# Kernel optimization log

Measured on AMD Instinct MI355X. Metric: run time of the kernel, lower is better.

The kernel has to match this reference:

```python
import jax, jax.numpy as jnp
import numpy as np

IN, H, NE, ED = 2048, 1024, 1024, 8
BETA = 0.001
LN_EPS = 1e-5


def _ln(x, g, b):
    m = jnp.mean(x, axis=-1, keepdims=True)
    v = jnp.var(x, axis=-1, keepdims=True)
    return (x - m) / jnp.sqrt(v + LN_EPS) * g + b


def setup_inputs() -> dict:
    key = jax.random.key(0)
    ks = jax.random.split(key, 10)

    def lin(k, fan_in, fan_out):
        lim = 1.0 / np.sqrt(fan_in)
        k1, k2 = jax.random.split(k)
        W = jax.random.uniform(k1, (fan_in, fan_out), minval=-lim, maxval=lim, dtype=jnp.float32)
        b = jax.random.uniform(k2, (fan_out,), minval=-lim, maxval=lim, dtype=jnp.float32)
        return W, b

    x = jax.random.normal(ks[0], (4096, IN), dtype=jnp.float32)
    r = ED ** -0.5
    codebook = jax.random.uniform(ks[1], (NE, ED), minval=-r, maxval=r, dtype=jnp.float32)
    W0, b0 = lin(ks[2], IN, H)
    W1, b1 = lin(ks[3], H, H)
    W2, b2 = lin(ks[4], H, H)
    W3, b3 = lin(ks[5], H, H)
    W4, b4 = lin(ks[6], H, H)
    W5, b5 = lin(ks[7], H, IN)
    ones = jnp.ones((H,), jnp.float32)
    zeros = jnp.zeros((H,), jnp.float32)
    return {
        "x": x, "codebook": codebook,
        "W0": W0, "b0": b0, "g0": ones, "be0": zeros,
        "W1": W1, "b1": b1, "g1": ones, "be1": zeros,
        "W2": W2, "b2": b2, "g2": ones, "be2": zeros,
        "W3": W3, "b3": b3, "g3": ones, "be3": zeros,
        "W4": W4, "b4": b4, "g4": ones, "be4": zeros,
        "W5": W5, "b5": b5,
    }


def reference(x, codebook,
              W0, b0, g0, be0,
              W1, b1, g1, be1,
              W2, b2, g2, be2,
              W3, b3, g3, be3,
              W4, b4, g4, be4,
              W5, b5):
    # encoder: Linear -> LN -> ReLU (x2) -> Linear -> LN
    h = jax.nn.relu(_ln(x @ W0 + b0, g0, be0))
    h = jax.nn.relu(_ln(h @ W1 + b1, g1, be1))
    z = _ln(h @ W2 + b2, g2, be2)                      # [B, H]

    # vector quantize: cdist^2 -> argmin -> gather, straight-through
    zf = z.reshape(-1, ED)                             # [B*H/ED, ED]
    d = (jnp.sum(zf * zf, axis=1, keepdims=True)
         + jnp.sum(codebook * codebook, axis=1)
         - 2.0 * zf @ codebook.T)                      # [B*H/ED, NE]
    idx = jnp.argmin(d, axis=1)
    z_q = codebook[idx].reshape(z.shape)
    loss = (jnp.mean((jax.lax.stop_gradient(z_q) - z) ** 2)
            + BETA * jnp.mean((z_q - jax.lax.stop_gradient(z)) ** 2))
    z_q = z + jax.lax.stop_gradient(z_q - z)

    # decoder: ReLU -> Linear -> LN (x2 with ReLU) -> ReLU -> Linear
    h = jax.nn.relu(z_q)
    h = jax.nn.relu(_ln(h @ W3 + b3, g3, be3))
    h = jax.nn.relu(_ln(h @ W4 + b4, g4, be4))
    x_hat = h @ W5 + b5
    return x_hat, loss
```

## Files before the change

kernel.cpp:

```cpp
#include <hip/hip_runtime.h>

namespace {

constexpr int BATCH = 4096;
constexpr int DIN   = 2048;
constexpr int HID   = 1024;
constexpr int NEMB  = 1024;
constexpr int EDIM  = 8;
constexpr float LN_EPS = 1e-5f;
constexpr float BETA   = 0.001f;

typedef __attribute__((ext_vector_type(8))) short bf16x8;
typedef __attribute__((ext_vector_type(4))) float f32x4;

__device__ inline unsigned short f2bf(float f) {
  unsigned int x = __float_as_uint(f);
  x += 0x7FFFu + ((x >> 16) & 1u);
  return (unsigned short)(x >> 16);
}
__device__ inline void gl16(const void* g, void* l) {
  __builtin_amdgcn_global_load_lds(
      (const __attribute__((address_space(1))) unsigned int*)g,
      (__attribute__((address_space(3))) unsigned int*)l, 16, 0, 0);
}

__global__ __launch_bounds__(256) void gemm_f32_sk(
    const float* __restrict__ A, const float* __restrict__ B,
    float* __restrict__ P, int M, int N, int K)
{
  constexpr int BM = 128, BN = 128, BK = 16;
  __shared__ float As[BK][BM + 4];
  __shared__ float Bs[BK][BN];
  const int t  = threadIdx.x;
  const int tx = t & 15, ty = t >> 4;
  const int bm = blockIdx.y * BM, bn = blockIdx.x * BN;
  const int Kh = K >> 1, kbeg = blockIdx.z * Kh;
  float* Pz = P + (size_t)blockIdx.z * M * N;

  const int a_m = t >> 1, a_k = (t & 1) << 3;
  const int b_k = t >> 4, b_n = (t & 15) << 3;

  const float* Ap = A + (size_t)(bm + a_m) * K + kbeg + a_k;
  const float* Bp = B + (size_t)(kbeg + b_k) * N + (bn + b_n);

  float acc[8][8] = {};

  for (int k0 = 0; k0 < Kh; k0 += BK) {
    float4 av0 = *(const float4*)(Ap + k0);
    float4 av1 = *(const float4*)(Ap + k0 + 4);
    float4 bv0 = *(const float4*)(Bp + (size_t)k0 * N);
    float4 bv1 = *(const float4*)(Bp + (size_t)k0 * N + 4);
    __syncthreads();
    As[a_k + 0][a_m] = av0.x;
    As[a_k + 1][a_m] = av0.y;
    As[a_k + 2][a_m] = av0.z;
    As[a_k + 3][a_m] = av0.w;
    As[a_k + 4][a_m] = av1.x;
    As[a_k + 5][a_m] = av1.y;
    As[a_k + 6][a_m] = av1.z;
    As[a_k + 7][a_m] = av1.w;
    *(float4*)&Bs[b_k][b_n]     = bv0;
    *(float4*)&Bs[b_k][b_n + 4] = bv1;
    __syncthreads();

    float part[8][8] = {};
#pragma unroll
    for (int k = 0; k < BK; ++k) {
      float a[8], b[8];
      *(float4*)(a)     = *(const float4*)&As[k][ty * 8];
      *(float4*)(a + 4) = *(const float4*)&As[k][ty * 8 + 4];
      *(float4*)(b)     = *(const float4*)&Bs[k][tx * 8];
      *(float4*)(b + 4) = *(const float4*)&Bs[k][tx * 8 + 4];
#pragma unroll
      for (int i = 0; i < 8; ++i)
#pragma unroll
        for (int j = 0; j < 8; ++j)
          part[i][j] = fmaf(a[i], b[j], part[i][j]);
    }
#pragma unroll
    for (int i = 0; i < 8; ++i)
#pragma unroll
      for (int j = 0; j < 8; ++j)
        acc[i][j] += part[i][j];
  }

#pragma unroll
  for (int i = 0; i < 8; ++i) {
    float* Pr = Pz + (size_t)(bm + ty * 8 + i) * N + bn + tx * 8;
    *(float4*)(Pr)     = *(float4*)&acc[i][0];
    *(float4*)(Pr + 4) = *(float4*)&acc[i][4];
  }
}

template<bool RELU>
__global__ __launch_bounds__(256) void ln_sk(
    const float* __restrict__ P0, const float* __restrict__ P1,
    const float* __restrict__ bias, float* __restrict__ Y,
    const float* __restrict__ g, const float* __restrict__ be)
{
  const int t = threadIdx.x;
  const size_t base = (size_t)blockIdx.x * HID + t * 4;
  float4 p0 = *(const float4*)(P0 + base);
  float4 p1 = *(const float4*)(P1 + base);
  float4 bb = *(const float4*)(bias + t * 4);
  float4 v;
  v.x = (p0.x + p1.x) + bb.x;
  v.y = (p0.y + p1.y) + bb.y;
  v.z = (p0.z + p1.z) + bb.z;
  v.w = (p0.w + p1.w) + bb.w;
  float s = v.x + v.y + v.z + v.w;
  float q = v.x * v.x + v.y * v.y + v.z * v.z + v.w * v.w;
#pragma unroll
  for (int off = 32; off > 0; off >>= 1) {
    s += __shfl_down(s, off);
    q += __shfl_down(q, off);
  }
  __shared__ float ls[4], lq[4];
  if ((t & 63) == 0) { ls[t >> 6] = s; lq[t >> 6] = q; }
  __syncthreads();
  s = ls[0] + ls[1] + ls[2] + ls[3];
  q = lq[0] + lq[1] + lq[2] + lq[3];
  const float mean = s * (1.0f / HID);
  const float var  = q * (1.0f / HID) - mean * mean;
  const float rstd = rsqrtf(var + LN_EPS);
  float4 gv = *(const float4*)(g + t * 4);
  float4 bv = *(const float4*)(be + t * 4);
  float4 o;
  o.x = (v.x - mean) * rstd * gv.x + bv.x;
  o.y = (v.y - mean) * rstd * gv.y + bv.y;
  o.z = (v.z - mean) * rstd * gv.z + bv.z;
  o.w = (v.w - mean) * rstd * gv.w + bv.w;
  if (RELU) {
    o.x = fmaxf(o.x, 0.0f); o.y = fmaxf(o.y, 0.0f);
    o.z = fmaxf(o.z, 0.0f); o.w = fmaxf(o.w, 0.0f);
  }
  *(float4*)(Y + base) = o;
}

__global__ __launch_bounds__(256) void gemm_mfma(
    const unsigned short* __restrict__ Ah, const unsigned short* __restrict__ Bh,
    const float* __restrict__ bias, float* __restrict__ C,
    int M, int N, int K)
{
  constexpr int BM = 128, BN = 64, BK = 64;
  __shared__ unsigned short lds[(BM + BN) * BK];
  const int t = threadIdx.x, l = t & 63, w = t >> 6;
  const int wr = w >> 1, wc = w & 1;
  const int m0 = blockIdx.y * BM, n0 = blockIdx.x * BN;
  const int NT = K / BK;

  const int AHo = 0, BHo = BM * BK * 2;

  const int srow = t >> 3, scol = t & 7;
  size_t aoff[4]; int adst[4];
#pragma unroll
  for (int i = 0; i < 4; ++i) {
    int r = srow + 32 * i;
    aoff[i] = (size_t)(m0 + r) * K + ((scol ^ (r & 7)) << 3);
    adst[i] = r * 128 + scol * 16;
  }
  size_t boff[2]; int bdst[2];
#pragma unroll
  for (int i = 0; i < 2; ++i) {
    int r = srow + 32 * i;
    boff[i] = (size_t)(n0 + r) * K + ((scol ^ (r & 7)) << 3);
    bdst[i] = r * 128 + scol * 16;
  }
  char* lc = (char*)lds;

  auto GLOAD = [&](int tk) {
    const size_t k0 = (size_t)tk * BK;
#pragma unroll
    for (int i = 0; i < 4; ++i) gl16(Ah + aoff[i] + k0, lc + AHo + adst[i]);
#pragma unroll
    for (int i = 0; i < 2; ++i) gl16(Bh + boff[i] + k0, lc + BHo + bdst[i]);
  };

  f32x4 acc[4][2];
#pragma unroll
  for (int i = 0; i < 4; ++i)
#pragma unroll
    for (int j = 0; j < 2; ++j) acc[i][j] = 0.0f;

  const int l15 = l & 15, kb0 = l >> 4;
  const int swz = (l15 & 7) << 4;
  int arow[4], brow[2];
#pragma unroll
  for (int fm = 0; fm < 4; ++fm) arow[fm] = (wr * 64 + fm * 16 + l15) * 128;
#pragma unroll
  for (int fn = 0; fn < 2; ++fn) brow[fn] = (wc * 32 + fn * 16 + l15) * 128;

  GLOAD(0);
  for (int tk = 0; tk < NT; ++tk) {
    __syncthreads();
    const char* p = (const char*)lds;
#pragma unroll
    for (int kh = 0; kh < 2; ++kh) {
      const int kby = (kh * 64 + kb0 * 16) ^ swz;
      bf16x8 af[4], bf2[2];
#pragma unroll
      for (int fm = 0; fm < 4; ++fm)
        af[fm] = *(const bf16x8*)(p + AHo + arow[fm] + kby);
#pragma unroll
      for (int fn = 0; fn < 2; ++fn)
        bf2[fn] = *(const bf16x8*)(p + BHo + brow[fn] + kby);
#pragma unroll
      for (int fm = 0; fm < 4; ++fm)
#pragma unroll
        for (int fn = 0; fn < 2; ++fn)
          acc[fm][fn] = __builtin_amdgcn_mfma_f32_16x16x32_bf16(
              af[fm], bf2[fn], acc[fm][fn], 0, 0, 0);
    }
    __syncthreads();
    if (tk + 1 < NT) GLOAD(tk + 1);
  }

  const int rb = (l >> 4) * 4;
#pragma unroll
  for (int fn = 0; fn < 2; ++fn) {
    const int n = n0 + wc * 32 + fn * 16 + l15;
    const float bv = bias[n];
#pragma unroll
    for (int fm = 0; fm < 4; ++fm) {
      const int m = m0 + wr * 64 + fm * 16 + rb;
      float* Cp = C + (size_t)m * N + n;
#pragma unroll
      for (int ri = 0; ri < 4; ++ri)
        Cp[(size_t)ri * N] = acc[fm][fn][ri] + bv;
    }
  }
}

__global__ __launch_bounds__(256) void conv_w_t(
    const float* __restrict__ W, unsigned short* __restrict__ Wt, int K, int N)
{
  __shared__ float tile[32][33];
  const int tx = threadIdx.x & 31, ty = threadIdx.x >> 5;
  const int n0 = blockIdx.x * 32, k0 = blockIdx.y * 32;
#pragma unroll
  for (int r = ty; r < 32; r += 8)
    tile[r][tx] = W[(size_t)(k0 + r) * N + n0 + tx];
  __syncthreads();
#pragma unroll
  for (int r = ty; r < 32; r += 8)
    Wt[(size_t)(n0 + r) * K + k0 + tx] = f2bf(tile[tx][r]);
}

template<bool RELU>
__global__ __launch_bounds__(256) void ln_act(
    const float* __restrict__ X, unsigned short* __restrict__ Y,
    const float* __restrict__ g, const float* __restrict__ be)
{
  const int t = threadIdx.x;
  const size_t base = (size_t)blockIdx.x * HID + t * 4;
  float4 v = *(const float4*)(X + base);
  float s = v.x + v.y + v.z + v.w;
  float q = v.x * v.x + v.y * v.y + v.z * v.z + v.w * v.w;
#pragma unroll
  for (int off = 32; off > 0; off >>= 1) {
    s += __shfl_down(s, off);
    q += __shfl_down(q, off);
  }
  __shared__ float ls[4], lq[4];
  if ((t & 63) == 0) { ls[t >> 6] = s; lq[t >> 6] = q; }
  __syncthreads();
  s = ls[0] + ls[1] + ls[2] + ls[3];
  q = lq[0] + lq[1] + lq[2] + lq[3];
  const float mean = s * (1.0f / HID);
  const float var  = q * (1.0f / HID) - mean * mean;
  const float rstd = rsqrtf(var + LN_EPS);
  float4 gv = *(const float4*)(g + t * 4);
  float4 bv = *(const float4*)(be + t * 4);
  float4 o;
  o.x = (v.x - mean) * rstd * gv.x + bv.x;
  o.y = (v.y - mean) * rstd * gv.y + bv.y;
  o.z = (v.z - mean) * rstd * gv.z + bv.z;
  o.w = (v.w - mean) * rstd * gv.w + bv.w;
  if (RELU) {
    o.x = fmaxf(o.x, 0.0f); o.y = fmaxf(o.y, 0.0f);
    o.z = fmaxf(o.z, 0.0f); o.w = fmaxf(o.w, 0.0f);
  }
  ushort4 u = { f2bf(o.x), f2bf(o.y), f2bf(o.z), f2bf(o.w) };
  *(ushort4*)(Y + base) = u;
}

__global__ __launch_bounds__(256) void vq_kernel(
    const float* __restrict__ Z, const float* __restrict__ CB,
    unsigned short* __restrict__ ZQb, float* __restrict__ partial)
{
  __shared__ float e[NEMB][EDIM];
  __shared__ float qn[NEMB];
  const int t = threadIdx.x;
  for (int i = t; i < NEMB * EDIM / 4; i += 256)
    ((float4*)&e[0][0])[i] = ((const float4*)CB)[i];
  __syncthreads();
  for (int i = t; i < NEMB; i += 256) {
    float s = 0.0f;
#pragma unroll
    for (int j = 0; j < EDIM; ++j) s += e[i][j] * e[i][j];
    qn[i] = 0.5f * s;
  }
  __syncthreads();

  constexpr int R = 2;
  size_t sv[R];
  float z[R][EDIM];
#pragma unroll
  for (int r = 0; r < R; ++r) {
    sv[r] = (size_t)blockIdx.x * 512 + t + 256 * r;
    *(float4*)(z[r])     = *(const float4*)(Z + sv[r] * EDIM);
    *(float4*)(z[r] + 4) = *(const float4*)(Z + sv[r] * EDIM + 4);
  }

  float b1[R], b2[R];
  int   i1[R], i2[R];
#pragma unroll
  for (int r = 0; r < R; ++r) { b1[r] = 1e30f; b2[r] = 1e30f; i1[r] = 0; i2[r] = 0; }

  for (int i = 0; i < NEMB; i += 4) {
    const float4 qv = *(const float4*)&qn[i];
#pragma unroll
    for (int u = 0; u < 4; ++u) {
      const float4 e0 = *(const float4*)&e[i + u][0];
      const float4 e1 = *(const float4*)&e[i + u][4];
      const float q = (u == 0) ? qv.x : (u == 1) ? qv.y : (u == 2) ? qv.z : qv.w;
      const int ii = i + u;
#pragma unroll
      for (int r = 0; r < R; ++r) {
        float d = q;
        d = fmaf(-z[r][0], e0.x, d);
        d = fmaf(-z[r][1], e0.y, d);
        d = fmaf(-z[r][2], e0.z, d);
        d = fmaf(-z[r][3], e0.w, d);
        d = fmaf(-z[r][4], e1.x, d);
        d = fmaf(-z[r][5], e1.y, d);
        d = fmaf(-z[r][6], e1.z, d);
        d = fmaf(-z[r][7], e1.w, d);
        const bool lt1 = d < b1[r];
        const bool lt2 = d < b2[r];
        i2[r] = lt1 ? i1[r] : (lt2 ? ii : i2[r]);
        b2[r] = fminf(fmaxf(d, b1[r]), b2[r]);
        if (lt1) { b1[r] = d; i1[r] = ii; }
      }
    }
  }

  double lsum = 0.0;
#pragma unroll
  for (int r = 0; r < R; ++r) {
    if (b2[r] - b1[r] < 1e-3f) {
      double d1 = 0.0, d2 = 0.0;
#pragma unroll
      for (int j = 0; j < EDIM; ++j) {
        double f1 = (double)z[r][j] - (double)e[i1[r]][j];
        double f2 = (double)z[r][j] - (double)e[i2[r]][j];
        d1 += f1 * f1; d2 += f2 * f2;
      }
      if (d2 < d1 || (d2 == d1 && i2[r] < i1[r])) i1[r] = i2[r];
    }
    double lq = 0.0;
#pragma unroll
    for (int j = 0; j < EDIM; ++j) {
      double diff = (double)z[r][j] - (double)e[i1[r]][j];
      lq += diff * diff;
    }
    lsum += lq;

    float o[EDIM];
#pragma unroll
    for (int j = 0; j < EDIM; ++j) o[j] = fmaxf(e[i1[r]][j], 0.0f);
    uint4 pk;
    pk.x = (unsigned)f2bf(o[0]) | ((unsigned)f2bf(o[1]) << 16);
    pk.y = (unsigned)f2bf(o[2]) | ((unsigned)f2bf(o[3]) << 16);
    pk.z = (unsigned)f2bf(o[4]) | ((unsigned)f2bf(o[5]) << 16);
    pk.w = (unsigned)f2bf(o[6]) | ((unsigned)f2bf(o[7]) << 16);
    *(uint4*)(ZQb + sv[r] * EDIM) = pk;
  }

#pragma unroll
  for (int off = 32; off > 0; off >>= 1) lsum += __shfl_down(lsum, off);
  __shared__ double lsh[4];
  if ((t & 63) == 0) lsh[t >> 6] = lsum;
  __syncthreads();
  if (t == 0) partial[blockIdx.x] = (float)(lsh[0] + lsh[1] + lsh[2] + lsh[3]);
}

__global__ __launch_bounds__(256) void loss_finalize(
    const float* __restrict__ partial, float* __restrict__ out)
{
  const int t = threadIdx.x;
  double s = 0.0;
  for (int i = t; i < 1024; i += 256) s += (double)partial[i];
#pragma unroll
  for (int off = 32; off > 0; off >>= 1) s += __shfl_down(s, off);
  __shared__ double ls[4];
  if ((t & 63) == 0) ls[t >> 6] = s;
  __syncthreads();
  if (t == 0) {
    double total = ls[0] + ls[1] + ls[2] + ls[3];
    out[0] = (float)(total * (1.0 + (double)BETA) / (double)((size_t)BATCH * HID));
  }
}

}

extern "C" void kernel_launch(void* const* d_in, const int* in_sizes, int n_in,
                              void* d_out, int out_size, void* d_ws, size_t ws_size,
                              hipStream_t stream)
{
  const float* x   = (const float*)d_in[0];
  const float* cb  = (const float*)d_in[1];
  const float* W0  = (const float*)d_in[2];
  const float* b0  = (const float*)d_in[3];
  const float* g0  = (const float*)d_in[4];
  const float* be0 = (const float*)d_in[5];
  const float* W1  = (const float*)d_in[6];
  const float* b1  = (const float*)d_in[7];
  const float* g1  = (const float*)d_in[8];
  const float* be1 = (const float*)d_in[9];
  const float* W2  = (const float*)d_in[10];
  const float* b2  = (const float*)d_in[11];
  const float* g2  = (const float*)d_in[12];
  const float* be2 = (const float*)d_in[13];
  const float* W3  = (const float*)d_in[14];
  const float* b3  = (const float*)d_in[15];
  const float* g3  = (const float*)d_in[16];
  const float* be3 = (const float*)d_in[17];
  const float* W4  = (const float*)d_in[18];
  const float* b4  = (const float*)d_in[19];
  const float* g4  = (const float*)d_in[20];
  const float* be4 = (const float*)d_in[21];
  const float* W5  = (const float*)d_in[22];
  const float* b5  = (const float*)d_in[23];
  float* out = (float*)d_out;

  char* ws = (char*)d_ws;
  constexpr size_t MB = 1024 * 1024;
  float* C32 = (float*)ws;
  float* Q   = (float*)(ws + 16 * MB);
  unsigned short* Qb  = (unsigned short*)(ws + 16 * MB);
  unsigned short* W3H = (unsigned short*)(ws + 24 * MB);
  unsigned short* W4H = (unsigned short*)(ws + 26 * MB);
  unsigned short* W5H = (unsigned short*)(ws + 28 * MB);
  float* partial = (float*)(ws + 32 * MB);
  float* P0 = (float*)d_out;
  float* P1 = (float*)((char*)d_out + 16 * MB);
  float* Z  = (float*)((char*)d_out + 16 * MB);

  dim3 blk(256);
  dim3 gSK(HID / 128, BATCH / 128, 2);
  dim3 gDH(HID / 64, BATCH / 128);
  dim3 gDO(DIN / 64, BATCH / 128);

  gemm_f32_sk<<<gSK, blk, 0, stream>>>(x, W0, P0, BATCH, HID, DIN);
  ln_sk<true><<<dim3(BATCH), blk, 0, stream>>>(P0, P1, b0, Q, g0, be0);
  gemm_f32_sk<<<gSK, blk, 0, stream>>>(Q, W1, P0, BATCH, HID, HID);
  ln_sk<true><<<dim3(BATCH), blk, 0, stream>>>(P0, P1, b1, Q, g1, be1);
  gemm_f32_sk<<<gSK, blk, 0, stream>>>(Q, W2, P0, BATCH, HID, HID);
  ln_sk<false><<<dim3(BATCH), blk, 0, stream>>>(P0, P1, b2, Z, g2, be2);

  conv_w_t<<<dim3(HID / 32, HID / 32), blk, 0, stream>>>(W3, W3H, HID, HID);
  conv_w_t<<<dim3(HID / 32, HID / 32), blk, 0, stream>>>(W4, W4H, HID, HID);
  conv_w_t<<<dim3(DIN / 32, HID / 32), blk, 0, stream>>>(W5, W5H, HID, DIN);

  vq_kernel<<<dim3(1024), blk, 0, stream>>>(Z, cb, Qb, partial);

  gemm_mfma<<<gDH, blk, 0, stream>>>(Qb, W3H, b3, C32, BATCH, HID, HID);
  ln_act<true><<<dim3(BATCH), blk, 0, stream>>>(C32, Qb, g3, be3);
  gemm_mfma<<<gDH, blk, 0, stream>>>(Qb, W4H, b4, C32, BATCH, HID, HID);
  ln_act<true><<<dim3(BATCH), blk, 0, stream>>>(C32, Qb, g4, be4);
  gemm_mfma<<<gDO, blk, 0, stream>>>(Qb, W5H, b5, out, BATCH, DIN, HID);

  loss_finalize<<<dim3(1), blk, 0, stream>>>(partial, out + (size_t)BATCH * DIN);
}
```

Baseline: 816.8 us.

## Use 3-way split-K for fp32 encoder GEMMs and halve VQ shared memory

The fp32 encoder GEMMs now split K three ways instead of two. The grid goes from 512 to 768 blocks, which gives better wave fill on 256 CUs, and the third partial is written to the C32 workspace; the LayerNorm kernels now sum three partials. The VQ kernel loads the codebook in two halves so it needs half the LDS, which raises occupancy, and it fetches the chosen codewords from global memory for the loss and output. The cost is extra partial-buffer traffic and extra barriers in the VQ kernel.

```diff
diff --git a/kernel.cpp b/kernel.cpp
--- a/kernel.cpp
+++ b/kernel.cpp
@@ -26,7 +26,8 @@
 
 __global__ __launch_bounds__(256) void gemm_f32_sk(
     const float* __restrict__ A, const float* __restrict__ B,
-    float* __restrict__ P, int M, int N, int K)
+    float* __restrict__ P0, float* __restrict__ P1, float* __restrict__ P2,
+    int M, int N, int K)
 {
   constexpr int BM = 128, BN = 128, BK = 16;
   __shared__ float As[BK][BM + 4];
@@ -34,8 +35,12 @@
   const int t  = threadIdx.x;
   const int tx = t & 15, ty = t >> 4;
   const int bm = blockIdx.y * BM, bn = blockIdx.x * BN;
-  const int Kh = K >> 1, kbeg = blockIdx.z * Kh;
-  float* Pz = P + (size_t)blockIdx.z * M * N;
+  const int zz = blockIdx.z;
+  const int ntile = K >> 4, q = ntile / 3, rr = ntile % 3;
+  const int myt  = q + (zz < rr ? 1 : 0);
+  const int kbeg = (zz * q + (zz < rr ? zz : rr)) << 4;
+  const int Kh   = myt << 4;
+  float* Pz = (zz == 0) ? P0 : (zz == 1) ? P1 : P2;
 
   const int a_m = t >> 1, a_k = (t & 1) << 3;
   const int b_k = t >> 4, b_n = (t & 15) << 3;
@@ -93,21 +98,23 @@
 }
 
 template<bool RELU>
-__global__ __launch_bounds__(256) void ln_sk(
+__global__ __launch_bounds__(256) void ln_sk3(
     const float* __restrict__ P0, const float* __restrict__ P1,
-    const float* __restrict__ bias, float* __restrict__ Y,
+    const float* __restrict__ P2, const float* __restrict__ bias,
+    float* __restrict__ Y,
     const float* __restrict__ g, const float* __restrict__ be)
 {
   const int t = threadIdx.x;
   const size_t base = (size_t)blockIdx.x * HID + t * 4;
   float4 p0 = *(const float4*)(P0 + base);
   float4 p1 = *(const float4*)(P1 + base);
+  float4 p2 = *(const float4*)(P2 + base);
   float4 bb = *(const float4*)(bias + t * 4);
   float4 v;
-  v.x = (p0.x + p1.x) + bb.x;
-  v.y = (p0.y + p1.y) + bb.y;
-  v.z = (p0.z + p1.z) + bb.z;
-  v.w = (p0.w + p1.w) + bb.w;
+  v.x = ((p0.x + p1.x) + p2.x) + bb.x;
+  v.y = ((p0.y + p1.y) + p2.y) + bb.y;
+  v.z = ((p0.z + p1.z) + p2.z) + bb.z;
+  v.w = ((p0.w + p1.w) + p2.w) + bb.w;
   float s = v.x + v.y + v.z + v.w;
   float q = v.x * v.x + v.y * v.y + v.z * v.z + v.w * v.w;
 #pragma unroll
@@ -288,19 +295,10 @@
     const float* __restrict__ Z, const float* __restrict__ CB,
     unsigned short* __restrict__ ZQb, float* __restrict__ partial)
 {
-  __shared__ float e[NEMB][EDIM];
-  __shared__ float qn[NEMB];
+  constexpr int HN = NEMB / 2;
+  __shared__ float e[HN][EDIM];
+  __shared__ float qn[HN];
   const int t = threadIdx.x;
-  for (int i = t; i < NEMB * EDIM / 4; i += 256)
-    ((float4*)&e[0][0])[i] = ((const float4*)CB)[i];
-  __syncthreads();
-  for (int i = t; i < NEMB; i += 256) {
-    float s = 0.0f;
-#pragma unroll
-    for (int j = 0; j < EDIM; ++j) s += e[i][j] * e[i][j];
-    qn[i] = 0.5f * s;
-  }
-  __syncthreads();
 
   constexpr int R = 2;
   size_t sv[R];
@@ -317,30 +315,45 @@
 #pragma unroll
   for (int r = 0; r < R; ++r) { b1[r] = 1e30f; b2[r] = 1e30f; i1[r] = 0; i2[r] = 0; }
 
-  for (int i = 0; i < NEMB; i += 4) {
-    const float4 qv = *(const float4*)&qn[i];
-#pragma unroll
-    for (int u = 0; u < 4; ++u) {
-      const float4 e0 = *(const float4*)&e[i + u][0];
-      const float4 e1 = *(const float4*)&e[i + u][4];
-      const float q = (u == 0) ? qv.x : (u == 1) ? qv.y : (u == 2) ? qv.z : qv.w;
-      const int ii = i + u;
-#pragma unroll
-      for (int r = 0; r < R; ++r) {
-        float d = q;
-        d = fmaf(-z[r][0], e0.x, d);
-        d = fmaf(-z[r][1], e0.y, d);
-        d = fmaf(-z[r][2], e0.z, d);
-        d = fmaf(-z[r][3], e0.w, d);
-        d = fmaf(-z[r][4], e1.x, d);
-        d = fmaf(-z[r][5], e1.y, d);
-        d = fmaf(-z[r][6], e1.z, d);
-        d = fmaf(-z[r][7], e1.w, d);
-        const bool lt1 = d < b1[r];
-        const bool lt2 = d < b2[r];
-        i2[r] = lt1 ? i1[r] : (lt2 ? ii : i2[r]);
-        b2[r] = fminf(fmaxf(d, b1[r]), b2[r]);
-        if (lt1) { b1[r] = d; i1[r] = ii; }
+  for (int half = 0; half < 2; ++half) {
+    if (half) __syncthreads();
+    for (int i = t; i < HN * EDIM / 4; i += 256)
+      ((float4*)&e[0][0])[i] = ((const float4*)(CB + (size_t)half * HN * EDIM))[i];
+    __syncthreads();
+    for (int i = t; i < HN; i += 256) {
+      float s = 0.0f;
+#pragma unroll
+      for (int j = 0; j < EDIM; ++j) s += e[i][j] * e[i][j];
+      qn[i] = 0.5f * s;
+    }
+    __syncthreads();
+
+    const int ibase = half * HN;
+    for (int i = 0; i < HN; i += 4) {
+      const float4 qv = *(const float4*)&qn[i];
+#pragma unroll
+      for (int u = 0; u < 4; ++u) {
+        const float4 e0 = *(const float4*)&e[i + u][0];
+        const float4 e1 = *(const float4*)&e[i + u][4];
+        const float q = (u == 0) ? qv.x : (u == 1) ? qv.y : (u == 2) ? qv.z : qv.w;
+        const int ii = ibase + i + u;
+#pragma unroll
+        for (int r = 0; r < R; ++r) {
+          float d = q;
+          d = fmaf(-z[r][0], e0.x, d);
+          d = fmaf(-z[r][1], e0.y, d);
+          d = fmaf(-z[r][2], e0.z, d);
+          d = fmaf(-z[r][3], e0.w, d);
+          d = fmaf(-z[r][4], e1.x, d);
+          d = fmaf(-z[r][5], e1.y, d);
+          d = fmaf(-z[r][6], e1.z, d);
+          d = fmaf(-z[r][7], e1.w, d);
+          const bool lt1 = d < b1[r];
+          const bool lt2 = d < b2[r];
+          i2[r] = lt1 ? i1[r] : (lt2 ? ii : i2[r]);
+          b2[r] = fminf(fmaxf(d, b1[r]), b2[r]);
+          if (lt1) { b1[r] = d; i1[r] = ii; }
+        }
       }
     }
   }
@@ -348,32 +361,38 @@
   double lsum = 0.0;
 #pragma unroll
   for (int r = 0; r < R; ++r) {
+    float c1[EDIM], c2[EDIM];
+    *(float4*)(c1)     = *(const float4*)(CB + (size_t)i1[r] * EDIM);
+    *(float4*)(c1 + 4) = *(const float4*)(CB + (size_t)i1[r] * EDIM + 4);
     if (b2[r] - b1[r] < 1e-3f) {
+      *(float4*)(c2)     = *(const float4*)(CB + (size_t)i2[r] * EDIM);
+      *(float4*)(c2 + 4) = *(const float4*)(CB + (size_t)i2[r] * EDIM + 4);
       double d1 = 0.0, d2 = 0.0;
 #pragma unroll
       for (int j = 0; j < EDIM; ++j) {
-        double f1 = (double)z[r][j] - (double)e[i1[r]][j];
-        double f2 = (double)z[r][j] - (double)e[i2[r]][j];
+        double f1 = (double)z[r][j] - (double)c1[j];
+        double f2 = (double)z[r][j] - (double)c2[j];
         d1 += f1 * f1; d2 += f2 * f2;
       }
-      if (d2 < d1 || (d2 == d1 && i2[r] < i1[r])) i1[r] = i2[r];
+      if (d2 < d1 || (d2 == d1 && i2[r] < i1[r])) {
+        i1[r] = i2[r];
+#pragma unroll
+        for (int j = 0; j < EDIM; ++j) c1[j] = c2[j];
+      }
     }
     double lq = 0.0;
 #pragma unroll
     for (int j = 0; j < EDIM; ++j) {
-      double diff = (double)z[r][j] - (double)e[i1[r]][j];
+      double diff = (double)z[r][j] - (double)c1[j];
       lq += diff * diff;
     }
     lsum += lq;
 
-    float o[EDIM];
-#pragma unroll
-    for (int j = 0; j < EDIM; ++j) o[j] = fmaxf(e[i1[r]][j], 0.0f);
     uint4 pk;
-    pk.x = (unsigned)f2bf(o[0]) | ((unsigned)f2bf(o[1]) << 16);
-    pk.y = (unsigned)f2bf(o[2]) | ((unsigned)f2bf(o[3]) << 16);
-    pk.z = (unsigned)f2bf(o[4]) | ((unsigned)f2bf(o[5]) << 16);
-    pk.w = (unsigned)f2bf(o[6]) | ((unsigned)f2bf(o[7]) << 16);
+    pk.x = (unsigned)f2bf(fmaxf(c1[0], 0.0f)) | ((unsigned)f2bf(fmaxf(c1[1], 0.0f)) << 16);
+    pk.y = (unsigned)f2bf(fmaxf(c1[2], 0.0f)) | ((unsigned)f2bf(fmaxf(c1[3], 0.0f)) << 16);
+    pk.z = (unsigned)f2bf(fmaxf(c1[4], 0.0f)) | ((unsigned)f2bf(fmaxf(c1[5], 0.0f)) << 16);
+    pk.w = (unsigned)f2bf(fmaxf(c1[6], 0.0f)) | ((unsigned)f2bf(fmaxf(c1[7], 0.0f)) << 16);
     *(uint4*)(ZQb + sv[r] * EDIM) = pk;
   }
 
@@ -448,16 +467,16 @@
   float* Z  = (float*)((char*)d_out + 16 * MB);
 
   dim3 blk(256);
-  dim3 gSK(HID / 128, BATCH / 128, 2);
+  dim3 gSK(HID / 128, BATCH / 128, 3);
   dim3 gDH(HID / 64, BATCH / 128);
   dim3 gDO(DIN / 64, BATCH / 128);
 
-  gemm_f32_sk<<<gSK, blk, 0, stream>>>(x, W0, P0, BATCH, HID, DIN);
-  ln_sk<true><<<dim3(BATCH), blk, 0, stream>>>(P0, P1, b0, Q, g0, be0);
-  gemm_f32_sk<<<gSK, blk, 0, stream>>>(Q, W1, P0, BATCH, HID, HID);
-  ln_sk<true><<<dim3(BATCH), blk, 0, stream>>>(P0, P1, b1, Q, g1, be1);
-  gemm_f32_sk<<<gSK, blk, 0, stream>>>(Q, W2, P0, BATCH, HID, HID);
-  ln_sk<false><<<dim3(BATCH), blk, 0, stream>>>(P0, P1, b2, Z, g2, be2);
+  gemm_f32_sk<<<gSK, blk, 0, stream>>>(x, W0, P0, P1, C32, BATCH, HID, DIN);
+  ln_sk3<true><<<dim3(BATCH), blk, 0, stream>>>(P0, P1, C32, b0, Q, g0, be0);
+  gemm_f32_sk<<<gSK, blk, 0, stream>>>(Q, W1, P0, P1, C32, BATCH, HID, HID);
+  ln_sk3<true><<<dim3(BATCH), blk, 0, stream>>>(P0, P1, C32, b1, Q, g1, be1);
+  gemm_f32_sk<<<gSK, blk, 0, stream>>>(Q, W2, P0, P1, C32, BATCH, HID, HID);
+  ln_sk3<false><<<dim3(BATCH), blk, 0, stream>>>(P0, P1, C32, b2, Z, g2, be2);
 
   conv_w_t<<<dim3(HID / 32, HID / 32), blk, 0, stream>>>(W3, W3H, HID, HID);
   conv_w_t<<<dim3(HID / 32, HID / 32), blk, 0, stream>>>(W4, W4H, HID, HID);
```

Measured after the change: 826.9 us. About the same (+1.2%).

## Halve VQ codebook LDS footprint and process one vector per thread

Applied to the files above, without the earlier changes.

The VQ kernel now stages the codebook in shared memory in two halves of 512 entries instead of all 1024. Each thread handles one vector instead of two, and the grid doubles to 2048 blocks. The final codeword values are read from global memory rather than LDS. The intent is lower LDS use per block (about 18KB instead of 36KB) and more parallelism, for higher occupancy in the distance-scan loop. In exchange, each block loads and normalises the codebook per half, adds extra barriers, and the loss partial reduction covers twice as many entries.

```diff
diff --git a/kernel.cpp b/kernel.cpp
--- a/kernel.cpp
+++ b/kernel.cpp
@@ -288,94 +288,91 @@
     const float* __restrict__ Z, const float* __restrict__ CB,
     unsigned short* __restrict__ ZQb, float* __restrict__ partial)
 {
-  __shared__ float e[NEMB][EDIM];
-  __shared__ float qn[NEMB];
+  constexpr int HN = NEMB / 2;
+  __shared__ float e[HN][EDIM];
+  __shared__ float qn[HN];
   const int t = threadIdx.x;
-  for (int i = t; i < NEMB * EDIM / 4; i += 256)
-    ((float4*)&e[0][0])[i] = ((const float4*)CB)[i];
-  __syncthreads();
-  for (int i = t; i < NEMB; i += 256) {
-    float s = 0.0f;
-#pragma unroll
-    for (int j = 0; j < EDIM; ++j) s += e[i][j] * e[i][j];
-    qn[i] = 0.5f * s;
-  }
-  __syncthreads();
-
-  constexpr int R = 2;
-  size_t sv[R];
-  float z[R][EDIM];
-#pragma unroll
-  for (int r = 0; r < R; ++r) {
-    sv[r] = (size_t)blockIdx.x * 512 + t + 256 * r;
-    *(float4*)(z[r])     = *(const float4*)(Z + sv[r] * EDIM);
-    *(float4*)(z[r] + 4) = *(const float4*)(Z + sv[r] * EDIM + 4);
-  }
-
-  float b1[R], b2[R];
-  int   i1[R], i2[R];
-#pragma unroll
-  for (int r = 0; r < R; ++r) { b1[r] = 1e30f; b2[r] = 1e30f; i1[r] = 0; i2[r] = 0; }
-
-  for (int i = 0; i < NEMB; i += 4) {
-    const float4 qv = *(const float4*)&qn[i];
-#pragma unroll
-    for (int u = 0; u < 4; ++u) {
-      const float4 e0 = *(const float4*)&e[i + u][0];
-      const float4 e1 = *(const float4*)&e[i + u][4];
-      const float q = (u == 0) ? qv.x : (u == 1) ? qv.y : (u == 2) ? qv.z : qv.w;
-      const int ii = i + u;
-#pragma unroll
-      for (int r = 0; r < R; ++r) {
+
+  const size_t sv = (size_t)blockIdx.x * 256 + t;
+  float z[EDIM];
+  *(float4*)(z)     = *(const float4*)(Z + sv * EDIM);
+  *(float4*)(z + 4) = *(const float4*)(Z + sv * EDIM + 4);
+
+  float b1 = 1e30f, b2 = 1e30f;
+  int   i1 = 0, i2 = 0;
+
+  for (int half = 0; half < 2; ++half) {
+    if (half) __syncthreads();
+    for (int i = t; i < HN * EDIM / 4; i += 256)
+      ((float4*)&e[0][0])[i] = ((const float4*)(CB + (size_t)half * HN * EDIM))[i];
+    __syncthreads();
+    for (int i = t; i < HN; i += 256) {
+      float s = 0.0f;
+#pragma unroll
+      for (int j = 0; j < EDIM; ++j) s += e[i][j] * e[i][j];
+      qn[i] = 0.5f * s;
+    }
+    __syncthreads();
+
+    const int ibase = half * HN;
+    for (int i = 0; i < HN; i += 4) {
+      const float4 qv = *(const float4*)&qn[i];
+#pragma unroll
+      for (int u = 0; u < 4; ++u) {
+        const float4 e0 = *(const float4*)&e[i + u][0];
+        const float4 e1 = *(const float4*)&e[i + u][4];
+        const float q = (u == 0) ? qv.x : (u == 1) ? qv.y : (u == 2) ? qv.z : qv.w;
+        const int ii = ibase + i + u;
         float d = q;
-        d = fmaf(-z[r][0], e0.x, d);
-        d = fmaf(-z[r][1], e0.y, d);
-        d = fmaf(-z[r][2], e0.z, d);
-        d = fmaf(-z[r][3], e0.w, d);
-        d = fmaf(-z[r][4], e1.x, d);
-        d = fmaf(-z[r][5], e1.y, d);
-        d = fmaf(-z[r][6], e1.z, d);
-        d = fmaf(-z[r][7], e1.w, d);
-        const bool lt1 = d < b1[r];
-        const bool lt2 = d < b2[r];
-        i2[r] = lt1 ? i1[r] : (lt2 ? ii : i2[r]);
-        b2[r] = fminf(fmaxf(d, b1[r]), b2[r]);
-        if (lt1) { b1[r] = d; i1[r] = ii; }
+        d = fmaf(-z[0], e0.x, d);
+        d = fmaf(-z[1], e0.y, d);
+        d = fmaf(-z[2], e0.z, d);
+        d = fmaf(-z[3], e0.w, d);
+        d = fmaf(-z[4], e1.x, d);
+        d = fmaf(-z[5], e1.y, d);
+        d = fmaf(-z[6], e1.z, d);
+        d = fmaf(-z[7], e1.w, d);
+        const bool lt1 = d < b1;
+        const bool lt2 = d < b2;
+        i2 = lt1 ? i1 : (lt2 ? ii : i2);
+        b2 = fminf(fmaxf(d, b1), b2);
+        if (lt1) { b1 = d; i1 = ii; }
       }
     }
   }
 
+  float c1[EDIM], c2[EDIM];
+  *(float4*)(c1)     = *(const float4*)(CB + (size_t)i1 * EDIM);
+  *(float4*)(c1 + 4) = *(const float4*)(CB + (size_t)i1 * EDIM + 4);
+  if (b2 - b1 < 1e-3f) {
+    *(float4*)(c2)     = *(const float4*)(CB + (size_t)i2 * EDIM);
+    *(float4*)(c2 + 4) = *(const float4*)(CB + (size_t)i2 * EDIM + 4);
+    double d1 = 0.0, d2 = 0.0;
+#pragma unroll
+    for (int j = 0; j < EDIM; ++j) {
+      double f1 = (double)z[j] - (double)c1[j];
+      double f2 = (double)z[j] - (double)c2[j];
+      d1 += f1 * f1; d2 += f2 * f2;
+    }
+    if (d2 < d1 || (d2 == d1 && i2 < i1)) {
+      i1 = i2;
+#pragma unroll
+      for (int j = 0; j < EDIM; ++j) c1[j] = c2[j];
+    }
+  }
   double lsum = 0.0;
 #pragma unroll
-  for (int r = 0; r < R; ++r) {
-    if (b2[r] - b1[r] < 1e-3f) {
-      double d1 = 0.0, d2 = 0.0;
-#pragma unroll
-      for (int j = 0; j < EDIM; ++j) {
-        double f1 = (double)z[r][j] - (double)e[i1[r]][j];
-        double f2 = (double)z[r][j] - (double)e[i2[r]][j];
-        d1 += f1 * f1; d2 += f2 * f2;
-      }
-      if (d2 < d1 || (d2 == d1 && i2[r] < i1[r])) i1[r] = i2[r];
-    }
-    double lq = 0.0;
-#pragma unroll
-    for (int j = 0; j < EDIM; ++j) {
-      double diff = (double)z[r][j] - (double)e[i1[r]][j];
-      lq += diff * diff;
-    }
-    lsum += lq;
-
-    float o[EDIM];
-#pragma unroll
-    for (int j = 0; j < EDIM; ++j) o[j] = fmaxf(e[i1[r]][j], 0.0f);
-    uint4 pk;
-    pk.x = (unsigned)f2bf(o[0]) | ((unsigned)f2bf(o[1]) << 16);
-    pk.y = (unsigned)f2bf(o[2]) | ((unsigned)f2bf(o[3]) << 16);
-    pk.z = (unsigned)f2bf(o[4]) | ((unsigned)f2bf(o[5]) << 16);
-    pk.w = (unsigned)f2bf(o[6]) | ((unsigned)f2bf(o[7]) << 16);
-    *(uint4*)(ZQb + sv[r] * EDIM) = pk;
-  }
+  for (int j = 0; j < EDIM; ++j) {
+    double diff = (double)z[j] - (double)c1[j];
+    lsum += diff * diff;
+  }
+
+  uint4 pk;
+  pk.x = (unsigned)f2bf(fmaxf(c1[0], 0.0f)) | ((unsigned)f2bf(fmaxf(c1[1], 0.0f)) << 16);
+  pk.y = (unsigned)f2bf(fmaxf(c1[2], 0.0f)) | ((unsigned)f2bf(fmaxf(c1[3], 0.0f)) << 16);
+  pk.z = (unsigned)f2bf(fmaxf(c1[4], 0.0f)) | ((unsigned)f2bf(fmaxf(c1[5], 0.0f)) << 16);
+  pk.w = (unsigned)f2bf(fmaxf(c1[6], 0.0f)) | ((unsigned)f2bf(fmaxf(c1[7], 0.0f)) << 16);
+  *(uint4*)(ZQb + sv * EDIM) = pk;
 
 #pragma unroll
   for (int off = 32; off > 0; off >>= 1) lsum += __shfl_down(lsum, off);
@@ -390,7 +387,7 @@
 {
   const int t = threadIdx.x;
   double s = 0.0;
-  for (int i = t; i < 1024; i += 256) s += (double)partial[i];
+  for (int i = t; i < 2048; i += 256) s += (double)partial[i];
 #pragma unroll
   for (int off = 32; off > 0; off >>= 1) s += __shfl_down(s, off);
   __shared__ double ls[4];
@@ -463,7 +460,7 @@
   conv_w_t<<<dim3(HID / 32, HID / 32), blk, 0, stream>>>(W4, W4H, HID, HID);
   conv_w_t<<<dim3(DIN / 32, HID / 32), blk, 0, stream>>>(W5, W5H, HID, DIN);
 
-  vq_kernel<<<dim3(1024), blk, 0, stream>>>(Z, cb, Qb, partial);
+  vq_kernel<<<dim3(2048), blk, 0, stream>>>(Z, cb, Qb, partial);
 
   gemm_mfma<<<gDH, blk, 0, stream>>>(Qb, W3H, b3, C32, BATCH, HID, HID);
   ln_act<true><<<dim3(BATCH), blk, 0, stream>>>(C32, Qb, g3, be3);
```

New measurement: 803.3 us. No clear change (-1.6%).
